# Performance work log

Hardware: AMD Instinct MI355X
Metric: run time of the kernel (lower is better)

## Reference

```python
import jax, jax.numpy as jnp
import numpy as np

N_NODES = 50000
DEG = 16           # constant out-degree per center node
CUTOFF = 5.0


def setup_inputs() -> dict:
    key = jax.random.key(0)
    k1, k2 = jax.random.split(key)
    # positions scaled so a meaningful fraction of edges exceed the cutoff
    pos = jax.random.normal(k1, (N_NODES, 3), dtype=jnp.float32) * 3.0
    row = jnp.repeat(jnp.arange(N_NODES, dtype=jnp.int32), DEG)      # [E]
    col = jax.random.randint(k2, (N_NODES * DEG,), 0, N_NODES, dtype=jnp.int32)
    edge_index = jnp.stack([row, col], axis=0)                        # [2, E]
    return {"pos": pos, "edge_index": edge_index}


def reference(pos, edge_index):
    """Padded, vectorized DimeNet-style triplet generation.

    Assumes constant degree: edge_index[0] == repeat(arange(N), DEG), so the
    neighbor list of node i is edge_index[1].reshape(N, DEG)[i]. Triplets are
    the [N, DEG, DEG] all-pairs grid; `mask` marks entries that the original
    Python-loop implementation would actually emit (both edges within cutoff,
    j-slot != k-slot).  Masked slots carry 0 for angles/distances.
    """
    num_nodes = pos.shape[0]
    deg = edge_index.shape[1] // num_nodes
    nb = edge_index[1].reshape(num_nodes, deg)          # [N, d] neighbor ids

    R1 = pos[nb] - pos[:, None, :]                      # [N, d, 3] i -> neighbor vectors
    edge_dist = jnp.linalg.norm(R1, axis=-1)            # [N, d]
    valid = edge_dist <= CUTOFF                         # cutoff filter per edge

    diag = jnp.eye(deg, dtype=bool)
    mask = valid[:, :, None] & valid[:, None, :] & ~diag  # [N, d, d]

    # angle(j, i, k) = atan2(|R1_j x R1_k|, R1_j . R1_k)
    dot = jnp.einsum('njc,nkc->njk', R1, R1)            # [N, d, d]
    cross = jnp.cross(R1[:, :, None, :], R1[:, None, :, :])  # [N, d, d, 3]
    cn2 = jnp.sum(cross * cross, axis=-1)
    cross_norm = jnp.sqrt(jnp.where(mask, cn2, 1.0))    # safe sqrt on padded slots
    angles = jnp.where(mask, jnp.arctan2(cross_norm, dot), 0.0)

    # |pos_j - pos_k| = |R1_j - R1_k|
    dvec = R1[:, :, None, :] - R1[:, None, :, :]
    d2 = jnp.sum(dvec * dvec, axis=-1)
    distances_jk = jnp.where(mask, jnp.sqrt(jnp.where(mask & (d2 > 0), d2, 1.0)), 0.0)

    shape3 = (num_nodes, deg, deg)
    id3_i = jnp.broadcast_to(jnp.arange(num_nodes, dtype=jnp.int32)[:, None, None], shape3).reshape(-1)
    id3_j = jnp.broadcast_to(nb[:, :, None], shape3).reshape(-1)
    id3_k = jnp.broadcast_to(nb[:, None, :], shape3).reshape(-1)

    return (id3_i, id3_j, id3_k,
            distances_jk.reshape(-1), angles.reshape(-1), mask.reshape(-1))
```

## Files before the change

kernel.cpp:

```cpp
#include <hip/hip_runtime.h>


#define DEG 16
#define NODES_PER_BLOCK 8
#define THREADS (NODES_PER_BLOCK * 64)
#define CUTOFF_F 5.0f

typedef float f32x4 __attribute__((ext_vector_type(4)));

__device__ __forceinline__ float fast_atan2_pos(float y, float x) {
    const float PI_F   = 3.14159274f;
    const float PIO2_F = 1.57079637f;
    const float ax = fabsf(x);
    const float mn = fminf(ax, y);
    const float mx = fmaxf(ax, y);
    const float a = (mx > 0.0f) ? __fdividef(mn, mx) : 0.0f;
    const float s = a * a;
    float r = fmaf(s, fmaf(s, fmaf(s, fmaf(s, 0.0208351f, -0.085133f),
                                   0.180141f), -0.3302995f), 0.9998660f);
    r *= a;
    if (y > ax)    r = PIO2_F - r;
    if (x < 0.0f)  r = PI_F - r;
    return r;
}

__global__ __launch_bounds__(THREADS) void triplet_kernel(
    const float* __restrict__ pos,
    const int* __restrict__ col_idx,
    float* __restrict__ out,
    int num_nodes, int P)
{
    __shared__ float sx[THREADS / 4], sy[THREADS / 4], sz[THREADS / 4];
    __shared__ float scolf[THREADS / 4];
    __shared__ int   sval[THREADS / 4];

    const int base = blockIdx.x * NODES_PER_BLOCK;
    const int tid = threadIdx.x;

    if (tid < NODES_PER_BLOCK * DEG) {
        int nl = tid >> 4;
        int slot = tid & 15;
        int node = base + nl;
        if (node < num_nodes) {
            int c = col_idx[node * DEG + slot];
            float px = pos[3 * node], py = pos[3 * node + 1], pz = pos[3 * node + 2];
            float rx = pos[3 * c]     - px;
            float ry = pos[3 * c + 1] - py;
            float rz = pos[3 * c + 2] - pz;
            float d = sqrtf(rx * rx + ry * ry + rz * rz);
            sx[tid] = rx; sy[tid] = ry; sz[tid] = rz;
            scolf[tid] = (float)c;
            sval[tid] = (d <= CUTOFF_F) ? 1 : 0;
        }
    }
    __syncthreads();

    const int w = tid >> 6;
    const int lane = tid & 63;
    const int node = base + w;
    if (node >= num_nodes) return;

    const int ofs = w * DEG;
    const int j = lane >> 2;
    const int k0 = (lane & 3) << 2;

    const float jx = sx[ofs + j], jy = sy[ofs + j], jz = sz[ofs + j];
    const int   jv = sval[ofs + j];
    const float jcolf = scolf[ofs + j];

    f32x4 o_k, o_d, o_a, o_m;

    #pragma unroll
    for (int q = 0; q < 4; ++q) {
        const int k = k0 + q;
        const float kx = sx[ofs + k], ky = sy[ofs + k], kz = sz[ofs + k];
        const int   kv = sval[ofs + k];
        const bool m = (jv != 0) && (kv != 0) && (j != k);

        const float dot = jx * kx + jy * ky + jz * kz;
        const float cx = jy * kz - jz * ky;
        const float cy = jz * kx - jx * kz;
        const float cz = jx * ky - jy * kx;
        const float cn2 = cx * cx + cy * cy + cz * cz;
        const float ang = m ? fast_atan2_pos(sqrtf(cn2), dot) : 0.0f;

        const float dx = jx - kx, dy = jy - ky, dz = jz - kz;
        const float d2 = dx * dx + dy * dy + dz * dz;
        const float dist = m ? sqrtf(d2 > 0.0f ? d2 : 1.0f) : 0.0f;

        o_k[q] = scolf[ofs + k];
        o_d[q] = dist;
        o_a[q] = ang;
        o_m[q] = m ? 1.0f : 0.0f;
    }

    const int idx = node * (DEG * DEG) + lane * 4;
    const float fi = (float)node;
    f32x4 o_i; o_i[0] = fi; o_i[1] = fi; o_i[2] = fi; o_i[3] = fi;
    f32x4 o_j; o_j[0] = jcolf; o_j[1] = jcolf; o_j[2] = jcolf; o_j[3] = jcolf;

    float* o0 = out + idx;
    *reinterpret_cast<f32x4*>(o0)         = o_i;
    *reinterpret_cast<f32x4*>(o0 + P)     = o_j;
    *reinterpret_cast<f32x4*>(o0 + 2 * P) = o_k;
    *reinterpret_cast<f32x4*>(o0 + 3 * P) = o_d;
    *reinterpret_cast<f32x4*>(o0 + 4 * P) = o_a;
    *reinterpret_cast<f32x4*>(o0 + 5 * P) = o_m;
}

extern "C" void kernel_launch(void* const* d_in, const int* in_sizes, int n_in,
                              void* d_out, int out_size, void* d_ws, size_t ws_size,
                              hipStream_t stream) {
    const float* pos = (const float*)d_in[0];
    const int* edge_index = (const int*)d_in[1];

    const int num_nodes = in_sizes[0] / 3;
    const int E = in_sizes[1] / 2;
    const int* col = edge_index + E;

    const int P = num_nodes * (DEG * DEG);
    const int blocks = (num_nodes + NODES_PER_BLOCK - 1) / NODES_PER_BLOCK;

    triplet_kernel<<<blocks, THREADS, 0, stream>>>(
        pos, col, (float*)d_out, num_nodes, P);
}
```

Measured before the change: 54.27 us.

## Stage results in LDS and write each output array contiguously per wave

```diff
diff --git a/kernel.cpp b/kernel.cpp
--- a/kernel.cpp
+++ b/kernel.cpp
@@ -30,9 +30,10 @@
     float* __restrict__ out,
     int num_nodes, int P)
 {
-    __shared__ float sx[THREADS / 4], sy[THREADS / 4], sz[THREADS / 4];
-    __shared__ float scolf[THREADS / 4];
-    __shared__ int   sval[THREADS / 4];
+    __shared__ float sx[128], sy[128], sz[128], scolf[128];
+    __shared__ int   sval[128];
+    __shared__ float sdist[NODES_PER_BLOCK * 256];
+    __shared__ float sang[NODES_PER_BLOCK * 256];
 
     const int base = blockIdx.x * NODES_PER_BLOCK;
     const int tid = threadIdx.x;
@@ -57,55 +58,75 @@
 
     const int w = tid >> 6;
     const int lane = tid & 63;
-    const int node = base + w;
-    if (node >= num_nodes) return;
+    {
+        const int node = base + w;
+        if (node < num_nodes) {
+            const int ofs = w * DEG;
+            const int j = lane >> 2;
+            const int k0 = (lane & 3) << 2;
 
-    const int ofs = w * DEG;
-    const int j = lane >> 2;
-    const int k0 = (lane & 3) << 2;
+            const float jx = sx[ofs + j], jy = sy[ofs + j], jz = sz[ofs + j];
+            const int   jv = sval[ofs + j];
 
-    const float jx = sx[ofs + j], jy = sy[ofs + j], jz = sz[ofs + j];
-    const int   jv = sval[ofs + j];
-    const float jcolf = scolf[ofs + j];
+            f32x4 o_d, o_a;
 
-    f32x4 o_k, o_d, o_a, o_m;
+            #pragma unroll
+            for (int q = 0; q < 4; ++q) {
+                const int k = k0 + q;
+                const float kx = sx[ofs + k], ky = sy[ofs + k], kz = sz[ofs + k];
+                const int   kv = sval[ofs + k];
+                const bool m = (jv != 0) && (kv != 0) && (j != k);
 
-    #pragma unroll
-    for (int q = 0; q < 4; ++q) {
-        const int k = k0 + q;
-        const float kx = sx[ofs + k], ky = sy[ofs + k], kz = sz[ofs + k];
-        const int   kv = sval[ofs + k];
-        const bool m = (jv != 0) && (kv != 0) && (j != k);
+                const float dot = jx * kx + jy * ky + jz * kz;
+                const float cx = jy * kz - jz * ky;
+                const float cy = jz * kx - jx * kz;
+                const float cz = jx * ky - jy * kx;
+                const float cn2 = cx * cx + cy * cy + cz * cz;
+                const float ang = m ? fast_atan2_pos(sqrtf(cn2), dot) : 0.0f;
 
-        const float dot = jx * kx + jy * ky + jz * kz;
-        const float cx = jy * kz - jz * ky;
-        const float cy = jz * kx - jx * kz;
-        const float cz = jx * ky - jy * kx;
-        const float cn2 = cx * cx + cy * cy + cz * cz;
-        const float ang = m ? fast_atan2_pos(sqrtf(cn2), dot) : 0.0f;
+                const float dx = jx - kx, dy = jy - ky, dz = jz - kz;
+                const float d2 = dx * dx + dy * dy + dz * dz;
+                const float dist = m ? sqrtf(d2 > 0.0f ? d2 : 1.0f) : 0.0f;
 
-        const float dx = jx - kx, dy = jy - ky, dz = jz - kz;
-        const float d2 = dx * dx + dy * dy + dz * dz;
-        const float dist = m ? sqrtf(d2 > 0.0f ? d2 : 1.0f) : 0.0f;
+                o_d[q] = dist;
+                o_a[q] = ang;
+            }
+            *reinterpret_cast<f32x4*>(&sdist[w * 256 + 4 * lane]) = o_d;
+            *reinterpret_cast<f32x4*>(&sang[w * 256 + 4 * lane])  = o_a;
+        }
+    }
+    __syncthreads();
 
-        o_k[q] = scolf[ofs + k];
-        o_d[q] = dist;
-        o_a[q] = ang;
-        o_m[q] = m ? 1.0f : 0.0f;
+    if (w < 6) {
+        float* const arr = out + w * P;
+        #pragma unroll
+        for (int c = 0; c < NODES_PER_BLOCK; ++c) {
+            const int node = base + c;
+            if (node >= num_nodes) break;
+            const int g = node * 256 + 4 * lane;
+            f32x4 v;
+            if (w == 0) {
+                const float fv = (float)node;
+                v[0] = fv; v[1] = fv; v[2] = fv; v[3] = fv;
+            } else if (w == 1) {
+                const float jv = scolf[c * 16 + (lane >> 2)];
+                v[0] = jv; v[1] = jv; v[2] = jv; v[3] = jv;
+            } else if (w == 2) {
+                v = *reinterpret_cast<const f32x4*>(&scolf[c * 16 + 4 * (lane & 3)]);
+            } else if (w == 3) {
+                v = *reinterpret_cast<const f32x4*>(&sdist[c * 256 + 4 * lane]);
+            } else if (w == 4) {
+                v = *reinterpret_cast<const f32x4*>(&sang[c * 256 + 4 * lane]);
+            } else {
+                const f32x4 d = *reinterpret_cast<const f32x4*>(&sdist[c * 256 + 4 * lane]);
+                v[0] = d[0] > 0.0f ? 1.0f : 0.0f;
+                v[1] = d[1] > 0.0f ? 1.0f : 0.0f;
+                v[2] = d[2] > 0.0f ? 1.0f : 0.0f;
+                v[3] = d[3] > 0.0f ? 1.0f : 0.0f;
+            }
+            *reinterpret_cast<f32x4*>(arr + g) = v;
+        }
     }
-
-    const int idx = node * (DEG * DEG) + lane * 4;
-    const float fi = (float)node;
-    f32x4 o_i; o_i[0] = fi; o_i[1] = fi; o_i[2] = fi; o_i[3] = fi;
-    f32x4 o_j; o_j[0] = jcolf; o_j[1] = jcolf; o_j[2] = jcolf; o_j[3] = jcolf;
-
-    float* o0 = out + idx;
-    *reinterpret_cast<f32x4*>(o0)         = o_i;
-    *reinterpret_cast<f32x4*>(o0 + P)     = o_j;
-    *reinterpret_cast<f32x4*>(o0 + 2 * P) = o_k;
-    *reinterpret_cast<f32x4*>(o0 + 3 * P) = o_d;
-    *reinterpret_cast<f32x4*>(o0 + 4 * P) = o_a;
-    *reinterpret_cast<f32x4*>(o0 + 5 * P) = o_m;
 }
 
 extern "C" void kernel_launch(void* const* d_in, const int* in_sizes, int n_in,
```

Result: slower. 58.42 us (+7.7%).
